# Kernel tuning notes

Measured on AMD Instinct MI355X. Metric: run time of the kernel, lower is better.

Reference implementation:

```python
import jax, jax.numpy as jnp
import numpy as np
import math

E = 500_000   # edges
N = 2_000     # nodes (small so duplicate (src,dst) pairs form real groups)
D = 128       # embedding_dim == n_heads*qkv_dim
H = 8         # heads
DK = 16       # qkv_dim
HH = 256      # hyper hidden
EMBD = 2      # hyper embd_dim
CLIP = 10.0   # tanh_clipping


def setup_inputs() -> dict:
    key = jax.random.key(0)
    ks = jax.random.split(key, 12)
    # shared_nodes: inverse indices of unique edge (src,dst) columns (reset() preprocessing)
    rng = np.random.default_rng(0)
    edge_indices = rng.integers(0, N, size=(2, E))
    _, inv = np.unique(edge_indices, axis=1, return_inverse=True)
    shared_nodes = jnp.asarray(inv.reshape(-1), dtype=jnp.int32)

    def lin(k, shape, fan_in):
        return jax.random.normal(k, shape, jnp.float32) / np.sqrt(fan_in)

    return {
        "pref": jax.random.uniform(ks[0], (2,), jnp.float32),
        "dists": jax.random.uniform(ks[1], (E, 2), jnp.float32),
        "edge_emb": jax.random.normal(ks[2], (E, D), jnp.float32),
        "shared_nodes": shared_nodes,
        "fc1_w": lin(ks[3], (HH, 2), 2), "fc1_b": jnp.zeros((HH,), jnp.float32),
        "fc2_w": lin(ks[4], (HH, HH), HH), "fc2_b": jnp.zeros((HH,), jnp.float32),
        "fc3_w": lin(ks[5], (2 * EMBD, HH), HH), "fc3_b": jnp.zeros((2 * EMBD,), jnp.float32),
        "wq_w": lin(ks[6], (D * H * DK, EMBD), EMBD),
        "wk_w": lin(ks[7], (D * H * DK, EMBD), EMBD),
    }


def reference(pref, dists, edge_emb, shared_nodes,
              fc1_w, fc1_b, fc2_w, fc2_b, fc3_w, fc3_b, wq_w, wk_w):
    # --- assign(pref): hypernetwork producing Wq, Wk (no activations, per source) ---
    h = pref @ fc1_w.T + fc1_b
    h = h @ fc2_w.T + fc2_b
    mid = h @ fc3_w.T + fc3_b                    # [4]
    Wq = (mid[:EMBD] @ wq_w.T).reshape(D, H * DK)
    Wk = (mid[EMBD:2 * EMBD] @ wk_w.T).reshape(D, H * DK)

    # --- reset(): scalarized distances + group means over shared edge groups ---
    d = pref[0] * dists[:, 0] + pref[1] * dists[:, 1]   # [E]
    n_edges = edge_emb.shape[0]
    seg = shared_nodes
    group_sums = jax.ops.segment_sum(edge_emb, seg, num_segments=n_edges)
    counts = jax.ops.segment_sum(jnp.ones((n_edges,), edge_emb.dtype), seg,
                                 num_segments=n_edges)
    group_means = group_sums / jnp.clip(counts, 1.0)[:, None]
    q = group_means[seg]                          # [E, D]

    # --- forward(): edge-wise multi-head dot score, tanh clip, group softmax ---
    fq = (q @ Wq.T).reshape(n_edges, H, DK)       # F.linear(q, Wq) (D == H*DK)
    fk = (edge_emb @ Wk.T).reshape(n_edges, H, DK)
    score = (fq * fk).sum(-1).mean(-1) / math.sqrt(D) - d / math.sqrt(2.0)
    score = CLIP * jnp.tanh(score)

    seg_max = jax.ops.segment_max(score, seg, num_segments=n_edges)
    ex = jnp.exp(score - seg_max[seg])
    denom = jax.ops.segment_sum(ex, seg, num_segments=n_edges)
    probs = ex / denom[seg]
    return probs[:, None]                         # [E, 1]
```

## Files before the change

### kernel.cpp

```cpp
#include <hip/hip_runtime.h>
#include <math.h>

#define DD 128
#define HHID 256
#define SLOTS 8

__global__ void k_build_M(const float* __restrict__ pref,
                          const float* __restrict__ fc1_w, const float* __restrict__ fc1_b,
                          const float* __restrict__ fc2_w, const float* __restrict__ fc2_b,
                          const float* __restrict__ fc3_w, const float* __restrict__ fc3_b,
                          const float* __restrict__ wq_w, const float* __restrict__ wk_w,
                          float* __restrict__ M_) {
    __shared__ float h1[HHID];
    __shared__ float h2[HHID];
    __shared__ float mid[4];
    int t = threadIdx.x;
    float p0 = pref[0], p1 = pref[1];
    h1[t] = fc1_w[t * 2 + 0] * p0 + fc1_w[t * 2 + 1] * p1 + fc1_b[t];
    __syncthreads();
    float acc = fc2_b[t];
    for (int i = 0; i < HHID; ++i) acc += fc2_w[t * HHID + i] * h1[i];
    h2[t] = acc;
    __syncthreads();
    if (t < 4) {
        float m = fc3_b[t];
        for (int i = 0; i < HHID; ++i) m += fc3_w[t * HHID + i] * h2[i];
        mid[t] = m;
    }
    __syncthreads();
    float m0 = mid[0], m1 = mid[1], m2 = mid[2], m3 = mid[3];
    int r = blockIdx.x * 2 + (t >> 7);
    int c = t & 127;
    const float scale = 0.011048543456f;
    float s = 0.f;
    for (int a = 0; a < DD; ++a) {
        float wq = wq_w[(a * DD + r) * 2 + 0] * m0 + wq_w[(a * DD + r) * 2 + 1] * m1;
        float wk = wk_w[(a * DD + c) * 2 + 0] * m2 + wk_w[(a * DD + c) * 2 + 1] * m3;
        s += wq * wk;
    }
    M_[r * DD + c] = s * scale;
}

__global__ void k_count_fill(const int* __restrict__ seg, unsigned* __restrict__ counts,
                             int* __restrict__ mem, int E_) {
    int e = blockIdx.x * blockDim.x + threadIdx.x;
    if (e >= E_) return;
    int g = seg[e];
    unsigned j = atomicAdd(&counts[g], 1u);
    if (j < SLOTS) mem[(size_t)g * SLOTS + j] = e;
}

__global__ void k_classify(const int* __restrict__ seg, const unsigned* __restrict__ counts,
                           int* __restrict__ glist, int* __restrict__ nctr,
                           float* __restrict__ out, int E_) {
    __shared__ int lcnt;
    __shared__ int lbase;
    int tid = blockIdx.x * blockDim.x + threadIdx.x;
    if (threadIdx.x == 0) lcnt = 0;
    __syncthreads();
    bool claim = false;
    int lpos = 0;
    if (tid < E_) {
        int g = seg[tid];
        if (counts[g] == 1u) out[tid] = 1.0f;
        claim = (counts[tid] >= 2u);
        if (claim) lpos = atomicAdd(&lcnt, 1);
    }
    __syncthreads();
    if (threadIdx.x == 0 && lcnt) lbase = atomicAdd(&nctr[1], lcnt);
    __syncthreads();
    if (claim) glist[lbase + lpos] = tid;
}

__global__ void k_mean(const int* __restrict__ glist, const int* __restrict__ nctr,
                       const unsigned* __restrict__ counts, const int* __restrict__ mem,
                       const float4* __restrict__ emb4, float4* __restrict__ gmean4) {
    int ng = nctr[1];
    int total = ng * 32;
    int stride = gridDim.x * blockDim.x;
    for (int idx = blockIdx.x * blockDim.x + threadIdx.x; idx < total; idx += stride) {
        int i = idx >> 5;
        int c4 = idx & 31;
        int g = glist[i];
        unsigned c = counts[g];
        int cm = (int)(c < (unsigned)SLOTS ? c : (unsigned)SLOTS);
        float4 s = make_float4(0.f, 0.f, 0.f, 0.f);
        for (int j = 0; j < cm; ++j) {
            int e = mem[(size_t)g * SLOTS + j];
            float4 v = emb4[(size_t)e * 32 + c4];
            s.x += v.x; s.y += v.y; s.z += v.z; s.w += v.w;
        }
        float inv = 1.0f / (float)c;
        gmean4[(size_t)i * 32 + c4] = make_float4(s.x * inv, s.y * inv, s.z * inv, s.w * inv);
    }
}

__global__ __launch_bounds__(256) void k_tg(const int* __restrict__ nctr,
                                            const float4* __restrict__ gmean4,
                                            const float4* __restrict__ M4,
                                            float4* __restrict__ gt4) {
    __shared__ float meanT[DD * 32];
    int t = threadIdx.x;
    int ng = nctr[1];
    int ntile = (ng + 31) >> 5;
    for (int tile = blockIdx.x; tile < ntile; tile += gridDim.x) {
        int i0 = tile * 32;
        {
            int gi = t & 31;
            int kq = t >> 5;
            int i = i0 + gi;
            if (i >= ng) i = ng - 1;
            for (int u = 0; u < 4; ++u) {
                float4 v = gmean4[(size_t)i * 32 + kq * 4 + u];
                int kbase = kq * 16 + u * 4;
                meanT[(kbase + 0) * 32 + gi] = v.x;
                meanT[(kbase + 1) * 32 + gi] = v.y;
                meanT[(kbase + 2) * 32 + gi] = v.z;
                meanT[(kbase + 3) * 32 + gi] = v.w;
            }
        }
        __syncthreads();
        int cseg = t & 31;
        int g4 = (t >> 5) * 4;
        float4 acc0 = make_float4(0.f, 0.f, 0.f, 0.f);
        float4 acc1 = acc0, acc2 = acc0, acc3 = acc0;
        #pragma unroll 4
        for (int k = 0; k < DD; ++k) {
            const float4* mrow = (const float4*)&meanT[k * 32 + g4];
            float4 mv = *mrow;
            float4 Mr = M4[k * 32 + cseg];
            acc0.x += mv.x * Mr.x; acc0.y += mv.x * Mr.y; acc0.z += mv.x * Mr.z; acc0.w += mv.x * Mr.w;
            acc1.x += mv.y * Mr.x; acc1.y += mv.y * Mr.y; acc1.z += mv.y * Mr.z; acc1.w += mv.y * Mr.w;
            acc2.x += mv.z * Mr.x; acc2.y += mv.z * Mr.y; acc2.z += mv.z * Mr.z; acc2.w += mv.z * Mr.w;
            acc3.x += mv.w * Mr.x; acc3.y += mv.w * Mr.y; acc3.z += mv.w * Mr.z; acc3.w += mv.w * Mr.w;
        }
        if (i0 + g4 + 0 < ng) gt4[(size_t)(i0 + g4 + 0) * 32 + cseg] = acc0;
        if (i0 + g4 + 1 < ng) gt4[(size_t)(i0 + g4 + 1) * 32 + cseg] = acc1;
        if (i0 + g4 + 2 < ng) gt4[(size_t)(i0 + g4 + 2) * 32 + cseg] = acc2;
        if (i0 + g4 + 3 < ng) gt4[(size_t)(i0 + g4 + 3) * 32 + cseg] = acc3;
        __syncthreads();
    }
}

__global__ void k_score(const int* __restrict__ glist, const int* __restrict__ nctr,
                        const unsigned* __restrict__ counts, const int* __restrict__ mem,
                        const float2* __restrict__ gt2, const float2* __restrict__ emb2,
                        const float2* __restrict__ dists2, const float* __restrict__ pref,
                        float* __restrict__ out) {
    int ng = nctr[1];
    int nw = (gridDim.x * blockDim.x) >> 6;
    int w = (blockIdx.x * blockDim.x + threadIdx.x) >> 6;
    int lane = threadIdx.x & 63;
    float p0 = pref[0], p1 = pref[1];
    for (int i = w; i < ng; i += nw) {
        int g = glist[i];
        unsigned c = counts[g];
        int cm = (int)(c < (unsigned)SLOTS ? c : (unsigned)SLOTS);
        float2 tv = gt2[(size_t)i * 64 + lane];
        float s_mine = 0.f;
        for (int j = 0; j < cm; ++j) {
            int e = mem[(size_t)g * SLOTS + j];
            float2 kv = emb2[(size_t)e * 64 + lane];
            float d = tv.x * kv.x + tv.y * kv.y;
            for (int off = 32; off; off >>= 1) d += __shfl_xor(d, off, 64);
            if (lane == j) s_mine = d;
        }
        int e_lane = -1;
        if (lane < cm) {
            e_lane = mem[(size_t)g * SLOTS + lane];
            float2 dd = dists2[e_lane];
            float de = p0 * dd.x + p1 * dd.y;
            s_mine = 10.0f * tanhf(s_mine - de * 0.7071067811865475f);
        }
        float v = (lane < cm) ? s_mine : -3.0e38f;
        for (int off = 32; off; off >>= 1) v = fmaxf(v, __shfl_xor(v, off, 64));
        float ex = (lane < cm) ? __expf(s_mine - v) : 0.f;
        float sm = ex;
        for (int off = 32; off; off >>= 1) sm += __shfl_xor(sm, off, 64);
        if (lane < cm) out[e_lane] = ex / sm;
    }
}

extern "C" void kernel_launch(void* const* d_in, const int* in_sizes, int n_in,
                              void* d_out, int out_size, void* d_ws, size_t ws_size,
                              hipStream_t stream) {
    const float* pref  = (const float*)d_in[0];
    const float* dists = (const float*)d_in[1];
    const float* emb   = (const float*)d_in[2];
    const int*   seg   = (const int*)d_in[3];
    const float* fc1_w = (const float*)d_in[4];
    const float* fc1_b = (const float*)d_in[5];
    const float* fc2_w = (const float*)d_in[6];
    const float* fc2_b = (const float*)d_in[7];
    const float* fc3_w = (const float*)d_in[8];
    const float* fc3_b = (const float*)d_in[9];
    const float* wq_w  = (const float*)d_in[10];
    const float* wk_w  = (const float*)d_in[11];
    int E_ = in_sizes[3];
    float* out = (float*)d_out;

    char* ws = (char*)d_ws;
    int*      nctr   = (int*)ws;
    unsigned* counts = (unsigned*)(ws + 256);
    size_t zero_bytes = 256 + (size_t)E_ * 4;
    char* p = ws + ((zero_bytes + 255) & ~(size_t)255);
    int*   glist = (int*)p;   p += ((size_t)E_ * 4 + 255) & ~(size_t)255;
    float* M_    = (float*)p; p += (size_t)DD * DD * 4;
    int*   mem   = (int*)p;   p += ((size_t)E_ * SLOTS * 4 + 255) & ~(size_t)255;
    float* gmean = (float*)p; p += (size_t)(E_ / 2) * DD * 4;
    float* gt    = (float*)p; p += (size_t)(E_ / 2) * DD * 4;
    if ((size_t)(p - ws) > ws_size) return;

    hipMemsetAsync(ws, 0, zero_bytes, stream);

    k_build_M<<<64, 256, 0, stream>>>(pref, fc1_w, fc1_b, fc2_w, fc2_b, fc3_w, fc3_b,
                                      wq_w, wk_w, M_);

    int tb = 256;
    int eb = (E_ + tb - 1) / tb;
    k_count_fill<<<eb, tb, 0, stream>>>(seg, counts, mem, E_);
    k_classify<<<eb, tb, 0, stream>>>(seg, counts, glist, nctr, out, E_);
    k_mean<<<1024, 256, 0, stream>>>(glist, nctr, counts, mem, (const float4*)emb,
                                     (float4*)gmean);
    k_tg<<<512, 256, 0, stream>>>(nctr, (const float4*)gmean, (const float4*)M_, (float4*)gt);
    k_score<<<1024, 256, 0, stream>>>(glist, nctr, counts, mem, (const float2*)gt,
                                      (const float2*)emb, (const float2*)dists, pref, out);
}
```

Baseline: 455.5 us.

## Fuse mean, projection and score kernels; merge count into hypernet setup

Merges the group-mean gather, the M projection and the per-group softmax score into one tiled kernel that keeps means and projected rows in shared memory. This removes the global round trips through the gmean and gt buffers. Counting now runs inside the same launch as the hypernetwork M build, and member-slot filling moves into classify, applied only to groups with more than one edge. The cost is a heavier fused kernel using 32KB of shared memory, which limits occupancy and serialises the phases within each block.

```diff
diff --git a/kernel.cpp b/kernel.cpp
--- a/kernel.cpp
+++ b/kernel.cpp
@@ -5,12 +5,18 @@
 #define HHID 256
 #define SLOTS 8
 
-__global__ void k_build_M(const float* __restrict__ pref,
-                          const float* __restrict__ fc1_w, const float* __restrict__ fc1_b,
-                          const float* __restrict__ fc2_w, const float* __restrict__ fc2_b,
-                          const float* __restrict__ fc3_w, const float* __restrict__ fc3_b,
-                          const float* __restrict__ wq_w, const float* __restrict__ wk_w,
-                          float* __restrict__ M_) {
+__global__ void k_setup(const float* __restrict__ pref,
+                        const float* __restrict__ fc1_w, const float* __restrict__ fc1_b,
+                        const float* __restrict__ fc2_w, const float* __restrict__ fc2_b,
+                        const float* __restrict__ fc3_w, const float* __restrict__ fc3_b,
+                        const float* __restrict__ wq_w, const float* __restrict__ wk_w,
+                        const int* __restrict__ seg, unsigned* __restrict__ counts,
+                        float* __restrict__ M_, int E_) {
+    if (blockIdx.x >= 64) {
+        int e = (int)(blockIdx.x - 64) * blockDim.x + threadIdx.x;
+        if (e < E_) atomicAdd(&counts[seg[e]], 1u);
+        return;
+    }
     __shared__ float h1[HHID];
     __shared__ float h2[HHID];
     __shared__ float mid[4];
@@ -41,16 +47,8 @@
     M_[r * DD + c] = s * scale;
 }
 
-__global__ void k_count_fill(const int* __restrict__ seg, unsigned* __restrict__ counts,
-                             int* __restrict__ mem, int E_) {
-    int e = blockIdx.x * blockDim.x + threadIdx.x;
-    if (e >= E_) return;
-    int g = seg[e];
-    unsigned j = atomicAdd(&counts[g], 1u);
-    if (j < SLOTS) mem[(size_t)g * SLOTS + j] = e;
-}
-
 __global__ void k_classify(const int* __restrict__ seg, const unsigned* __restrict__ counts,
+                           unsigned* __restrict__ slot, int* __restrict__ mem,
                            int* __restrict__ glist, int* __restrict__ nctr,
                            float* __restrict__ out, int E_) {
     __shared__ int lcnt;
@@ -62,7 +60,13 @@
     int lpos = 0;
     if (tid < E_) {
         int g = seg[tid];
-        if (counts[g] == 1u) out[tid] = 1.0f;
+        unsigned c = counts[g];
+        if (c == 1u) {
+            out[tid] = 1.0f;
+        } else {
+            unsigned j = atomicAdd(&slot[g], 1u);
+            if (j < SLOTS) mem[(size_t)g * SLOTS + j] = tid;
+        }
         claim = (counts[tid] >= 2u);
         if (claim) lpos = atomicAdd(&lcnt, 1);
     }
@@ -72,112 +76,113 @@
     if (claim) glist[lbase + lpos] = tid;
 }
 
-__global__ void k_mean(const int* __restrict__ glist, const int* __restrict__ nctr,
-                       const unsigned* __restrict__ counts, const int* __restrict__ mem,
-                       const float4* __restrict__ emb4, float4* __restrict__ gmean4) {
-    int ng = nctr[1];
-    int total = ng * 32;
-    int stride = gridDim.x * blockDim.x;
-    for (int idx = blockIdx.x * blockDim.x + threadIdx.x; idx < total; idx += stride) {
-        int i = idx >> 5;
-        int c4 = idx & 31;
-        int g = glist[i];
-        unsigned c = counts[g];
-        int cm = (int)(c < (unsigned)SLOTS ? c : (unsigned)SLOTS);
-        float4 s = make_float4(0.f, 0.f, 0.f, 0.f);
-        for (int j = 0; j < cm; ++j) {
-            int e = mem[(size_t)g * SLOTS + j];
-            float4 v = emb4[(size_t)e * 32 + c4];
-            s.x += v.x; s.y += v.y; s.z += v.z; s.w += v.w;
-        }
-        float inv = 1.0f / (float)c;
-        gmean4[(size_t)i * 32 + c4] = make_float4(s.x * inv, s.y * inv, s.z * inv, s.w * inv);
-    }
-}
-
-__global__ __launch_bounds__(256) void k_tg(const int* __restrict__ nctr,
-                                            const float4* __restrict__ gmean4,
-                                            const float4* __restrict__ M4,
-                                            float4* __restrict__ gt4) {
+__global__ __launch_bounds__(256) void k_fused(const int* __restrict__ glist,
+                                               const int* __restrict__ nctr,
+                                               const unsigned* __restrict__ counts,
+                                               const int* __restrict__ mem,
+                                               const float4* __restrict__ M4,
+                                               const float4* __restrict__ emb4,
+                                               const float2* __restrict__ emb2,
+                                               const float2* __restrict__ dists2,
+                                               const float* __restrict__ pref,
+                                               float* __restrict__ out) {
     __shared__ float meanT[DD * 32];
+    __shared__ float gtile[32 * DD];
     int t = threadIdx.x;
     int ng = nctr[1];
     int ntile = (ng + 31) >> 5;
+    float p0 = pref[0], p1 = pref[1];
     for (int tile = blockIdx.x; tile < ntile; tile += gridDim.x) {
         int i0 = tile * 32;
         {
             int gi = t & 31;
             int kq = t >> 5;
             int i = i0 + gi;
-            if (i >= ng) i = ng - 1;
-            for (int u = 0; u < 4; ++u) {
-                float4 v = gmean4[(size_t)i * 32 + kq * 4 + u];
-                int kbase = kq * 16 + u * 4;
-                meanT[(kbase + 0) * 32 + gi] = v.x;
-                meanT[(kbase + 1) * 32 + gi] = v.y;
-                meanT[(kbase + 2) * 32 + gi] = v.z;
-                meanT[(kbase + 3) * 32 + gi] = v.w;
+            float4 s0 = make_float4(0.f, 0.f, 0.f, 0.f), s1 = s0, s2 = s0, s3 = s0;
+            float inv = 0.f;
+            if (i < ng) {
+                int g = glist[i];
+                unsigned c = counts[g];
+                int cm = (int)(c < (unsigned)SLOTS ? c : (unsigned)SLOTS);
+                inv = 1.0f / (float)c;
+                for (int j = 0; j < cm; ++j) {
+                    int e = mem[(size_t)g * SLOTS + j];
+                    float4 v0 = emb4[(size_t)e * 32 + kq + 0];
+                    float4 v1 = emb4[(size_t)e * 32 + kq + 8];
+                    float4 v2 = emb4[(size_t)e * 32 + kq + 16];
+                    float4 v3 = emb4[(size_t)e * 32 + kq + 24];
+                    s0.x += v0.x; s0.y += v0.y; s0.z += v0.z; s0.w += v0.w;
+                    s1.x += v1.x; s1.y += v1.y; s1.z += v1.z; s1.w += v1.w;
+                    s2.x += v2.x; s2.y += v2.y; s2.z += v2.z; s2.w += v2.w;
+                    s3.x += v3.x; s3.y += v3.y; s3.z += v3.z; s3.w += v3.w;
+                }
             }
+            int k0 = (kq + 0) * 4, k1 = (kq + 8) * 4, k2 = (kq + 16) * 4, k3 = (kq + 24) * 4;
+            meanT[(k0 + 0) * 32 + gi] = s0.x * inv; meanT[(k0 + 1) * 32 + gi] = s0.y * inv;
+            meanT[(k0 + 2) * 32 + gi] = s0.z * inv; meanT[(k0 + 3) * 32 + gi] = s0.w * inv;
+            meanT[(k1 + 0) * 32 + gi] = s1.x * inv; meanT[(k1 + 1) * 32 + gi] = s1.y * inv;
+            meanT[(k1 + 2) * 32 + gi] = s1.z * inv; meanT[(k1 + 3) * 32 + gi] = s1.w * inv;
+            meanT[(k2 + 0) * 32 + gi] = s2.x * inv; meanT[(k2 + 1) * 32 + gi] = s2.y * inv;
+            meanT[(k2 + 2) * 32 + gi] = s2.z * inv; meanT[(k2 + 3) * 32 + gi] = s2.w * inv;
+            meanT[(k3 + 0) * 32 + gi] = s3.x * inv; meanT[(k3 + 1) * 32 + gi] = s3.y * inv;
+            meanT[(k3 + 2) * 32 + gi] = s3.z * inv; meanT[(k3 + 3) * 32 + gi] = s3.w * inv;
         }
         __syncthreads();
-        int cseg = t & 31;
-        int g4 = (t >> 5) * 4;
-        float4 acc0 = make_float4(0.f, 0.f, 0.f, 0.f);
-        float4 acc1 = acc0, acc2 = acc0, acc3 = acc0;
-        #pragma unroll 4
-        for (int k = 0; k < DD; ++k) {
-            const float4* mrow = (const float4*)&meanT[k * 32 + g4];
-            float4 mv = *mrow;
-            float4 Mr = M4[k * 32 + cseg];
-            acc0.x += mv.x * Mr.x; acc0.y += mv.x * Mr.y; acc0.z += mv.x * Mr.z; acc0.w += mv.x * Mr.w;
-            acc1.x += mv.y * Mr.x; acc1.y += mv.y * Mr.y; acc1.z += mv.y * Mr.z; acc1.w += mv.y * Mr.w;
-            acc2.x += mv.z * Mr.x; acc2.y += mv.z * Mr.y; acc2.z += mv.z * Mr.z; acc2.w += mv.z * Mr.w;
-            acc3.x += mv.w * Mr.x; acc3.y += mv.w * Mr.y; acc3.z += mv.w * Mr.z; acc3.w += mv.w * Mr.w;
-        }
-        if (i0 + g4 + 0 < ng) gt4[(size_t)(i0 + g4 + 0) * 32 + cseg] = acc0;
-        if (i0 + g4 + 1 < ng) gt4[(size_t)(i0 + g4 + 1) * 32 + cseg] = acc1;
-        if (i0 + g4 + 2 < ng) gt4[(size_t)(i0 + g4 + 2) * 32 + cseg] = acc2;
-        if (i0 + g4 + 3 < ng) gt4[(size_t)(i0 + g4 + 3) * 32 + cseg] = acc3;
+        {
+            int cseg = t & 31;
+            int g4 = (t >> 5) * 4;
+            float4 acc0 = make_float4(0.f, 0.f, 0.f, 0.f);
+            float4 acc1 = acc0, acc2 = acc0, acc3 = acc0;
+            #pragma unroll 4
+            for (int k = 0; k < DD; ++k) {
+                float4 mv = *(const float4*)&meanT[k * 32 + g4];
+                float4 Mr = M4[k * 32 + cseg];
+                acc0.x += mv.x * Mr.x; acc0.y += mv.x * Mr.y; acc0.z += mv.x * Mr.z; acc0.w += mv.x * Mr.w;
+                acc1.x += mv.y * Mr.x; acc1.y += mv.y * Mr.y; acc1.z += mv.y * Mr.z; acc1.w += mv.y * Mr.w;
+                acc2.x += mv.z * Mr.x; acc2.y += mv.z * Mr.y; acc2.z += mv.z * Mr.z; acc2.w += mv.z * Mr.w;
+                acc3.x += mv.w * Mr.x; acc3.y += mv.w * Mr.y; acc3.z += mv.w * Mr.z; acc3.w += mv.w * Mr.w;
+            }
+            *(float4*)&gtile[(g4 + 0) * DD + cseg * 4] = acc0;
+            *(float4*)&gtile[(g4 + 1) * DD + cseg * 4] = acc1;
+            *(float4*)&gtile[(g4 + 2) * DD + cseg * 4] = acc2;
+            *(float4*)&gtile[(g4 + 3) * DD + cseg * 4] = acc3;
+        }
         __syncthreads();
-    }
-}
-
-__global__ void k_score(const int* __restrict__ glist, const int* __restrict__ nctr,
-                        const unsigned* __restrict__ counts, const int* __restrict__ mem,
-                        const float2* __restrict__ gt2, const float2* __restrict__ emb2,
-                        const float2* __restrict__ dists2, const float* __restrict__ pref,
-                        float* __restrict__ out) {
-    int ng = nctr[1];
-    int nw = (gridDim.x * blockDim.x) >> 6;
-    int w = (blockIdx.x * blockDim.x + threadIdx.x) >> 6;
-    int lane = threadIdx.x & 63;
-    float p0 = pref[0], p1 = pref[1];
-    for (int i = w; i < ng; i += nw) {
-        int g = glist[i];
-        unsigned c = counts[g];
-        int cm = (int)(c < (unsigned)SLOTS ? c : (unsigned)SLOTS);
-        float2 tv = gt2[(size_t)i * 64 + lane];
-        float s_mine = 0.f;
-        for (int j = 0; j < cm; ++j) {
-            int e = mem[(size_t)g * SLOTS + j];
-            float2 kv = emb2[(size_t)e * 64 + lane];
-            float d = tv.x * kv.x + tv.y * kv.y;
-            for (int off = 32; off; off >>= 1) d += __shfl_xor(d, off, 64);
-            if (lane == j) s_mine = d;
-        }
-        int e_lane = -1;
-        if (lane < cm) {
-            e_lane = mem[(size_t)g * SLOTS + lane];
-            float2 dd = dists2[e_lane];
-            float de = p0 * dd.x + p1 * dd.y;
-            s_mine = 10.0f * tanhf(s_mine - de * 0.7071067811865475f);
-        }
-        float v = (lane < cm) ? s_mine : -3.0e38f;
-        for (int off = 32; off; off >>= 1) v = fmaxf(v, __shfl_xor(v, off, 64));
-        float ex = (lane < cm) ? __expf(s_mine - v) : 0.f;
-        float sm = ex;
-        for (int off = 32; off; off >>= 1) sm += __shfl_xor(sm, off, 64);
-        if (lane < cm) out[e_lane] = ex / sm;
+        {
+            int w = t >> 6;
+            int lane = t & 63;
+            for (int q = 0; q < 8; ++q) {
+                int gl = w * 8 + q;
+                int i = i0 + gl;
+                if (i >= ng) continue;
+                int g = glist[i];
+                unsigned c = counts[g];
+                int cm = (int)(c < (unsigned)SLOTS ? c : (unsigned)SLOTS);
+                float2 tv = *(const float2*)&gtile[gl * DD + 2 * lane];
+                float s_mine = 0.f;
+                for (int j = 0; j < cm; ++j) {
+                    int e = mem[(size_t)g * SLOTS + j];
+                    float2 kv = emb2[(size_t)e * 64 + lane];
+                    float d = tv.x * kv.x + tv.y * kv.y;
+                    for (int off = 32; off; off >>= 1) d += __shfl_xor(d, off, 64);
+                    if (lane == j) s_mine = d;
+                }
+                int e_lane = -1;
+                if (lane < cm) {
+                    e_lane = mem[(size_t)g * SLOTS + lane];
+                    float2 dd = dists2[e_lane];
+                    float de = p0 * dd.x + p1 * dd.y;
+                    s_mine = 10.0f * tanhf(s_mine - de * 0.7071067811865475f);
+                }
+                float v = (lane < cm) ? s_mine : -3.0e38f;
+                for (int off = 32; off; off >>= 1) v = fmaxf(v, __shfl_xor(v, off, 64));
+                float ex = (lane < cm) ? __expf(s_mine - v) : 0.f;
+                float sm = ex;
+                for (int off = 32; off; off >>= 1) sm += __shfl_xor(sm, off, 64);
+                if (lane < cm) out[e_lane] = ex / sm;
+            }
+        }
+        __syncthreads();
     }
 }
 
@@ -202,27 +207,22 @@
     char* ws = (char*)d_ws;
     int*      nctr   = (int*)ws;
     unsigned* counts = (unsigned*)(ws + 256);
-    size_t zero_bytes = 256 + (size_t)E_ * 4;
+    unsigned* slot   = (unsigned*)(ws + 256 + (size_t)E_ * 4);
+    size_t zero_bytes = 256 + (size_t)E_ * 8;
     char* p = ws + ((zero_bytes + 255) & ~(size_t)255);
     int*   glist = (int*)p;   p += ((size_t)E_ * 4 + 255) & ~(size_t)255;
     float* M_    = (float*)p; p += (size_t)DD * DD * 4;
-    int*   mem   = (int*)p;   p += ((size_t)E_ * SLOTS * 4 + 255) & ~(size_t)255;
-    float* gmean = (float*)p; p += (size_t)(E_ / 2) * DD * 4;
-    float* gt    = (float*)p; p += (size_t)(E_ / 2) * DD * 4;
+    int*   mem   = (int*)p;   p += (size_t)E_ * SLOTS * 4;
     if ((size_t)(p - ws) > ws_size) return;
 
     hipMemsetAsync(ws, 0, zero_bytes, stream);
-
-    k_build_M<<<64, 256, 0, stream>>>(pref, fc1_w, fc1_b, fc2_w, fc2_b, fc3_w, fc3_b,
-                                      wq_w, wk_w, M_);
 
     int tb = 256;
     int eb = (E_ + tb - 1) / tb;
-    k_count_fill<<<eb, tb, 0, stream>>>(seg, counts, mem, E_);
-    k_classify<<<eb, tb, 0, stream>>>(seg, counts, glist, nctr, out, E_);
-    k_mean<<<1024, 256, 0, stream>>>(glist, nctr, counts, mem, (const float4*)emb,
-                                     (float4*)gmean);
-    k_tg<<<512, 256, 0, stream>>>(nctr, (const float4*)gmean, (const float4*)M_, (float4*)gt);
-    k_score<<<1024, 256, 0, stream>>>(glist, nctr, counts, mem, (const float2*)gt,
-                                      (const float2*)emb, (const float2*)dists, pref, out);
-}
+    k_setup<<<64 + eb, tb, 0, stream>>>(pref, fc1_w, fc1_b, fc2_w, fc2_b, fc3_w, fc3_b,
+                                        wq_w, wk_w, seg, counts, M_, E_);
+    k_classify<<<eb, tb, 0, stream>>>(seg, counts, slot, mem, glist, nctr, out, E_);
+    k_fused<<<1024, 256, 0, stream>>>(glist, nctr, counts, mem, (const float4*)M_,
+                                      (const float4*)emb, (const float2*)emb,
+                                      (const float2*)dists, pref, out);
+}
```

New measurement: 438.7 us. 3.7% less time.
